# Kernel optimization log

Hardware: AMD Instinct MI355X
Metric: run time of the kernel (lower is better)

The kernel has to match this reference:

```python
import jax, jax.numpy as jnp
import numpy as np

R_, RD_, D_, C_ = 4, 64, 256, 64   # num_relations, relation_dim, input_dim, max_chains
B_, T_ = 32, 512
OUT = R_ * RD_                      # output_dim = num_relations * relation_dim
EPS = 1e-100                        # underflows to 0 in fp32, same as torch


def setup_inputs() -> dict:
    key = jax.random.key(0)
    ks = jax.random.split(key, 10)
    X = jax.random.normal(ks[0], (B_, T_, D_), jnp.float32)
    M = jax.random.randint(ks[1], (B_, T_), 0, 2, jnp.int32)
    Ei = jax.random.randint(ks[2], (B_, T_, C_), 0, 2, jnp.int32)
    Eo = jax.random.randint(ks[3], (B_, T_, C_), 0, 2, jnp.int32)
    Ri = jax.random.randint(ks[4], (B_, T_, C_), 0, R_, jnp.int32)
    Ro = jax.random.randint(ks[5], (B_, T_, C_), 0, R_, jnp.int32)
    W = jax.random.normal(ks[6], (D_, OUT), jnp.float32) * np.sqrt(6.0 / (D_ + OUT))
    U = jax.random.normal(ks[7], (OUT, OUT), jnp.float32) * np.sqrt(6.0 / (OUT + OUT))
    b = jnp.zeros((OUT,), jnp.float32)
    Watt = jax.random.normal(ks[8], (R_, D_), jnp.float32) * 0.1
    return dict(X=X, M=M, Ei=Ei, Eo=Eo, Ri=Ri, Ro=Ro, W=W, U=U, b=b, Watt=Watt)


def _forward(X, M, Ei, Eo, Ri, Ro, W, U, b, Watt):
    B = X.shape[0]
    dt = X.dtype
    # All three gates share the same W/U/b in the original module.
    Wstk = jnp.concatenate([W, W, W], axis=1)   # [D, 3*OUT]
    Ustk = jnp.concatenate([U, U, U], axis=1)   # [OUT, 3*OUT]

    # time-major
    Xre = jnp.transpose(X, (1, 0, 2))           # [T,B,D]
    Xpre = jnp.einsum('tbd,de->tbe', Xre, Wstk) # [T,B,3*OUT] precomputed input proj
    Mre = jnp.transpose(M, (1, 0))              # [T,B]
    Eire = jnp.transpose(Ei, (1, 0, 2))         # [T,B,C]
    Eore = jnp.transpose(Eo, (1, 0, 2))
    Rire = jnp.transpose(Ri, (1, 0, 2))
    Rore = jnp.transpose(Ro, (1, 0, 2))

    h0 = jnp.zeros((B, OUT), dt)
    m0 = jnp.zeros((B, C_, RD_), dt)

    def step(carry, inp):
        hprev, mprev = carry
        x, xp, m, ei, eo, ri, ro = inp
        # gather: one-hot over relations for each chain slot
        r1 = jax.nn.one_hot(ri, R_, dtype=dt)                 # [B,C,R]
        # attention over chains
        v = jnp.einsum('bcr,rd->bcd', r1, Watt)               # [B,C,D]
        actvs = jnp.einsum('bcd,bd->bc', v, x)                # [B,C]
        e = ei.astype(dt)
        am = jnp.exp(actvs) * e + EPS
        alphas = am / jnp.sum(am, axis=1, keepdims=True)      # [B,C]
        agg = jnp.transpose(alphas[:, :, None] * r1, (0, 2, 1))  # [B,R,C]
        prev = jnp.einsum('brc,bcd->brd', agg, mprev).reshape(B, OUT)  # [B,OUT]
        agg_out = jnp.sum(agg, axis=2)                        # [B,R]
        # fused GRU cell (shared weights across gates)
        h2h = prev @ Ustk                                     # [B,3*OUT]
        xr, xz, xh = xp[:, :OUT], xp[:, OUT:2 * OUT], xp[:, 2 * OUT:]
        hr, hz, hh = h2h[:, :OUT], h2h[:, OUT:2 * OUT], h2h[:, 2 * OUT:]
        rg = jax.nn.sigmoid(xr + hr + b)
        z = jax.nn.sigmoid(xz + hz + b)
        ht = jnp.tanh(xh + rg * hh + b)
        hnew = (1.0 - z) * prev + z * ht                      # [B,OUT]
        # scatter new hidden state back into per-chain memory
        hnew_r = hnew.reshape(B, R_, RD_)
        ro1 = jax.nn.one_hot(ro, R_, dtype=dt)                # [B,C,R]
        mnew = jnp.einsum('bcr,brd->bcd', ro1, hnew_r)        # [B,C,RD]
        mflt = m.astype(dt)[:, None]                          # [B,1]
        hout = (1.0 - mflt) * hprev + mflt * hnew
        eo_r = (mflt * eo.astype(dt))[:, :, None]             # [B,C,1]
        mout = (1.0 - eo_r) * mprev + eo_r * mnew
        return (hout, mout), (hout, mout, agg_out)

    _, (outs, mems, aggs) = jax.lax.scan(
        step, (h0, m0), (Xre, Xpre, Mre, Eire, Eore, Rire, Rore))
    return (jnp.transpose(outs, (1, 0, 2)),        # [B,T,OUT]
            jnp.transpose(mems, (1, 0, 2, 3)),     # [B,T,C,RD]
            jnp.transpose(aggs, (1, 0, 2)))        # [B,T,R]


def reference(X, M, Ei, Eo, Ri, Ro, W, U, b, Watt):
    return _forward(X, M, Ei, Eo, Ri, Ro, W, U, b, Watt)
```

## Files before the change

### kernel.cpp

```cpp
#include <hip/hip_runtime.h>

#define B_   32
#define T_   512
#define D_   256
#define C_   64
#define R_   4
#define RD_  64
#define OUT_ 256

__device__ __forceinline__ void bar_lds() {
  asm volatile("s_waitcnt lgkmcnt(0)" ::: "memory");
  __builtin_amdgcn_s_barrier();
  asm volatile("" ::: "memory");
}

template <int CTRL>
__device__ __forceinline__ float dpp_add(float v) {
  int s = __builtin_amdgcn_update_dpp(0, __float_as_int(v), CTRL, 0xF, 0xF, true);
  return v + __int_as_float(s);
}
__device__ __forceinline__ float row16_sum(float v) {
  v = dpp_add<0xB1>(v);
  v = dpp_add<0x4E>(v);
  v = dpp_add<0x141>(v);
  v = dpp_add<0x140>(v);
  return v;
}
__device__ __forceinline__ float rlane(float v, int l) {
  return __int_as_float(__builtin_amdgcn_readlane(__float_as_int(v), l));
}
__device__ __forceinline__ int rlane_i(int v, int l) {
  return __builtin_amdgcn_readlane(v, l);
}
__device__ __forceinline__ float wave_sum_dpp(float v) {
  const float r = row16_sum(v);
  return (rlane(r, 0) + rlane(r, 16)) + (rlane(r, 32) + rlane(r, 48));
}

__global__ __launch_bounds__(256) void xpre_kernel(const float* __restrict__ X,
                                                   const float* __restrict__ W,
                                                   float* __restrict__ XP) {
  __shared__ __align__(16) float xs[32][D_];
  const int j = threadIdx.x;
  const int row0 = blockIdx.x * 32;
  for (int k = 0; k < 32; ++k)
    xs[k][j] = X[(size_t)(row0 + k) * D_ + j];
  __syncthreads();
  float acc[32];
#pragma unroll
  for (int k = 0; k < 32; ++k) acc[k] = 0.f;
  for (int d4 = 0; d4 < D_ / 4; ++d4) {
    const float w0 = W[(d4 * 4 + 0) * OUT_ + j];
    const float w1 = W[(d4 * 4 + 1) * OUT_ + j];
    const float w2 = W[(d4 * 4 + 2) * OUT_ + j];
    const float w3 = W[(d4 * 4 + 3) * OUT_ + j];
#pragma unroll
    for (int k = 0; k < 32; ++k) {
      const float4 x4 = *(const float4*)&xs[k][d4 * 4];
      acc[k] = fmaf(x4.x, w0, fmaf(x4.y, w1, fmaf(x4.z, w2, fmaf(x4.w, w3, acc[k]))));
    }
  }
  for (int k = 0; k < 32; ++k)
    XP[(size_t)(row0 + k) * OUT_ + j] = acc[k];
}

__global__ __launch_bounds__(256) void attnK(const float* __restrict__ X,
                                             const int* __restrict__ Ri,
                                             const int* __restrict__ Ei,
                                             const float* __restrict__ Watt,
                                             float* __restrict__ walG,
                                             float* __restrict__ aggs) {
  const int wv = threadIdx.x >> 6;
  const int lane = threadIdx.x & 63;
  const size_t bt = (size_t)blockIdx.x * 4 + wv;
  const int r4 = lane >> 4, seg = lane & 15;

  float y = 0.f;
#pragma unroll
  for (int q = 0; q < 4; ++q) {
    const float4 wt = *(const float4*)&Watt[(r4 << 8) + (seg << 4) + (q << 2)];
    const float4 xv = *(const float4*)&X[bt * D_ + (seg << 4) + (q << 2)];
    y = fmaf(xv.x, wt.x, y);
    y = fmaf(xv.y, wt.y, y);
    y = fmaf(xv.z, wt.z, y);
    y = fmaf(xv.w, wt.w, y);
  }
  y = row16_sum(y);
  const float y0 = rlane(y, 0), y1 = rlane(y, 16);
  const float y2 = rlane(y, 32), y3 = rlane(y, 48);
  const int ric = Ri[bt * C_ + lane];
  const float eic = (float)Ei[bt * C_ + lane];
  float yv = (ric & 1) ? y1 : y0;
  const float yw = (ric & 1) ? y3 : y2;
  yv = (ric & 2) ? yw : yv;
  const float am = __expf(yv) * eic;
  const float tot = wave_sum_dpp(am);
  const float alpha = __fdividef(am, tot);

  const float w0 = (ric == 0) ? alpha : 0.f;
  const float w1 = (ric == 1) ? alpha : 0.f;
  const float w2 = (ric == 2) ? alpha : 0.f;
  const float w3 = (ric == 3) ? alpha : 0.f;
  walG[bt * 256 + 0 * C_ + lane] = w0;
  walG[bt * 256 + 1 * C_ + lane] = w1;
  walG[bt * 256 + 2 * C_ + lane] = w2;
  walG[bt * 256 + 3 * C_ + lane] = w3;
  const float s0 = wave_sum_dpp(w0);
  const float s1 = wave_sum_dpp(w1);
  const float s2 = wave_sum_dpp(w2);
  const float s3 = wave_sum_dpp(w3);
  if (lane == 0) {
    float4 v = {s0, s1, s2, s3};
    *(float4*)&aggs[bt * R_] = v;
  }
}

__global__ __launch_bounds__(256, 1) void gruA(
    const int* __restrict__ M, const int* __restrict__ Eo,
    const int* __restrict__ Ro, const float* __restrict__ U,
    const float* __restrict__ Bv, const float* __restrict__ XP,
    const float* __restrict__ walG, float* __restrict__ hbuf) {
  __shared__ __align__(16) float shp[4][256];
  __shared__ __align__(16) float pBred[4][256];
  __shared__ __align__(16) float sh_hnew[OUT_];
  __shared__ int sh_tl[T_];
  __shared__ int sh_nT;

  const int tid = threadIdx.x;
  const int lane = tid & 63;
  const int w = tid >> 6;
  const int b = blockIdx.x;
  const size_t bt0 = (size_t)b * T_;

  float ureg[256];
#pragma unroll
  for (int jj = 0; jj < 4; ++jj)
#pragma unroll
    for (int i = 0; i < 64; ++i)
      ureg[(jj << 6) + i] = U[(size_t)((w << 6) + i) * OUT_ + (jj << 6) + lane];
  const float breg = Bv[tid];

  float mtreg[16];
#pragma unroll
  for (int q = 0; q < 16; ++q) mtreg[q] = 0.f;

  if (tid < 64) {
    int base = 0;
    for (int ch = 0; ch < 8; ++ch) {
      const int mv = M[bt0 + (ch << 6) + lane];
      const unsigned long long mask = __ballot(mv != 0);
      if (mv) {
        const unsigned long long lt = ((lane == 63) ? ~0ull : ((1ull << (lane + 1)) - 1)) >> 1;
        sh_tl[base + __popcll(mask & lt)] = (ch << 6) + lane;
      }
      base += __popcll(mask);
    }
    if (lane == 0) sh_nT = base;
  }
  __syncthreads();
  const int nT = sh_nT;
  if (nT == 0) return;

  const int cwal = (w << 4) + (lane >> 2);
  const int croeo = (w << 4) + (lane & 15);
  float walS0 = 0.f, xpS0 = 0.f, walS1 = 0.f, xpS1 = 0.f;
  int roeoS0 = 0, roeoS1 = 0;
  {
    const int t0 = sh_tl[0];
    walS0 = walG[(bt0 + t0) * 256 + ((tid & 3) << 6) + cwal];
    xpS0 = XP[(bt0 + t0) * 256 + tid];
    roeoS0 = Ro[(bt0 + t0) * C_ + croeo] | (Eo[(bt0 + t0) * C_ + croeo] << 8);
  }
  if (nT > 1) {
    const int t1 = sh_tl[1];
    walS1 = walG[(bt0 + t1) * 256 + ((tid & 3) << 6) + cwal];
    xpS1 = XP[(bt0 + t1) * 256 + tid];
    roeoS1 = Ro[(bt0 + t1) * C_ + croeo] | (Eo[(bt0 + t1) * C_ + croeo] << 8);
  }

  auto do_step = [&](int k, float& walS, float& xpS, int& roeoS) {
    const size_t bt = bt0 + sh_tl[k];
    const int roeoCur = roeoS;

    float a0 = 0.f, a1 = 0.f, a2 = 0.f, a3 = 0.f;
#pragma unroll
    for (int q = 0; q < 16; ++q) {
      const float mq = mtreg[q];
      a0 = fmaf(rlane(walS, 4 * q + 0), mq, a0);
      a1 = fmaf(rlane(walS, 4 * q + 1), mq, a1);
      a2 = fmaf(rlane(walS, 4 * q + 2), mq, a2);
      a3 = fmaf(rlane(walS, 4 * q + 3), mq, a3);
    }
    shp[w][0 * 64 + lane] = a0;
    shp[w][1 * 64 + lane] = a1;
    shp[w][2 * 64 + lane] = a2;
    shp[w][3 * 64 + lane] = a3;
    bar_lds();

    const float prevX = ((shp[0][tid] + shp[1][tid]) +
                         (shp[2][tid] + shp[3][tid]));
    float p0 = 0.f, p1 = 0.f, p2 = 0.f, p3 = 0.f;
#pragma unroll
    for (int i = 0; i < 64; ++i) {
      const float pk = rlane(prevX, i);
      p0 = fmaf(pk, ureg[i], p0);
      p1 = fmaf(pk, ureg[64 + i], p1);
      p2 = fmaf(pk, ureg[128 + i], p2);
      p3 = fmaf(pk, ureg[192 + i], p3);
    }
    pBred[w][0 * 64 + lane] = p0;
    pBred[w][1 * 64 + lane] = p1;
    pBred[w][2 * 64 + lane] = p2;
    pBred[w][3 * 64 + lane] = p3;
    bar_lds();

    const float h2h = ((pBred[0][tid] + pBred[1][tid]) +
                       (pBred[2][tid] + pBred[3][tid]));
    const float g1 = xpS + h2h + breg;
    const float rg = 1.f / (1.f + __expf(-g1));
    const float targ = xpS + rg * h2h + breg;
    const float e2 = __expf(2.f * targ);
    const float ht = 1.f - 2.f / (e2 + 1.f);
    const float hn = (1.f - rg) * prevX + rg * ht;
    sh_hnew[tid] = hn;
    hbuf[bt * OUT_ + tid] = hn;
    if (k + 2 < nT) {
      const int t2 = sh_tl[k + 2];
      walS = walG[(bt0 + t2) * 256 + ((tid & 3) << 6) + cwal];
      xpS = XP[(bt0 + t2) * 256 + tid];
      roeoS = Ro[(bt0 + t2) * C_ + croeo] | (Eo[(bt0 + t2) * C_ + croeo] << 8);
    }
    bar_lds();

    const float h0 = sh_hnew[0 * 64 + lane];
    const float h1 = sh_hnew[1 * 64 + lane];
    const float h2 = sh_hnew[2 * 64 + lane];
    const float h3 = sh_hnew[3 * 64 + lane];
#pragma unroll
    for (int q = 0; q < 16; ++q) {
      const int re = rlane_i(roeoCur, q);
      const int ro = re & 0xFF;
      const float ha = (ro & 1) ? h1 : h0;
      const float hb = (ro & 1) ? h3 : h2;
      const float hs = (ro & 2) ? hb : ha;
      mtreg[q] = (re & 0x100) ? hs : mtreg[q];
    }
  };

  for (int k = 0; k < nT; k += 2) {
    do_step(k, walS0, xpS0, roeoS0);
    if (k + 1 < nT) do_step(k + 1, walS1, xpS1, roeoS1);
  }
}

__global__ __launch_bounds__(512) void memsB(const int* __restrict__ M,
                                             const int* __restrict__ Eo,
                                             const int* __restrict__ Ro,
                                             const float* __restrict__ hbuf,
                                             float* __restrict__ mems) {
  __shared__ int lastA[T_];
  const int tid = threadIdx.x;
  const int b = blockIdx.x >> 6;
  const int c = blockIdx.x & 63;
  const size_t bt0 = (size_t)b * T_;
  {
    const int upd = M[bt0 + tid] & Eo[(bt0 + tid) * C_ + c];
    lastA[tid] = upd ? tid : -1;
  }
  __syncthreads();
  for (int off = 1; off < T_; off <<= 1) {
    const int u = (tid >= off) ? lastA[tid - off] : -1;
    const int v = lastA[tid];
    __syncthreads();
    lastA[tid] = (u > v) ? u : v;
    __syncthreads();
  }
  const int d = tid & 63;
  const int t8 = tid >> 6;
  for (int tt = 0; tt < 64; ++tt) {
    const int t = (tt << 3) + t8;
    const int tau = lastA[t];
    float v = 0.f;
    if (tau >= 0) {
      const int rc = Ro[(bt0 + tau) * C_ + c];
      v = hbuf[(bt0 + tau) * OUT_ + (rc << 6) + d];
    }
    mems[((bt0 + t) * C_ + c) * RD_ + d] = v;
  }
}

__global__ __launch_bounds__(512) void outsC(const int* __restrict__ M,
                                             float* __restrict__ outs) {
  __shared__ int lastM[T_];
  const int tid = threadIdx.x;
  const int b = blockIdx.x;
  const size_t bt0 = (size_t)b * T_;
  lastM[tid] = M[bt0 + tid] ? tid : -1;
  __syncthreads();
  for (int off = 1; off < T_; off <<= 1) {
    const int u = (tid >= off) ? lastM[tid - off] : -1;
    const int v = lastM[tid];
    __syncthreads();
    lastM[tid] = (u > v) ? u : v;
    __syncthreads();
  }
  const int j = tid & 255;
  const int th = tid >> 8;
  for (int k = 0; k < 256; ++k) {
    const int t = 511 - (k << 1) - th;
    const int tau = lastM[t];
    const float v = (tau >= 0) ? outs[(bt0 + tau) * OUT_ + j] : 0.f;
    __syncthreads();
    outs[(bt0 + t) * OUT_ + j] = v;
  }
}

extern "C" void kernel_launch(void* const* d_in, const int* in_sizes, int n_in,
                              void* d_out, int out_size, void* d_ws, size_t ws_size,
                              hipStream_t stream) {
  const float* X = (const float*)d_in[0];
  const int* M = (const int*)d_in[1];
  const int* Ei = (const int*)d_in[2];
  const int* Eo = (const int*)d_in[3];
  const int* Ri = (const int*)d_in[4];
  const int* Ro = (const int*)d_in[5];
  const float* W = (const float*)d_in[6];
  const float* U = (const float*)d_in[7];
  const float* Bv = (const float*)d_in[8];
  const float* Watt = (const float*)d_in[9];

  float* outs = (float*)d_out;
  float* mems = outs + (size_t)B_ * T_ * OUT_;
  float* aggs = mems + (size_t)B_ * T_ * C_ * RD_;
  float* XP = (float*)d_ws;
  float* hbuf = outs;
  float* walG = mems;

  xpre_kernel<<<dim3(B_ * T_ / 32), dim3(256), 0, stream>>>(X, W, XP);
  attnK<<<dim3(B_ * T_ / 4), dim3(256), 0, stream>>>(X, Ri, Ei, Watt, walG, aggs);
  gruA<<<dim3(B_), dim3(256), 0, stream>>>(M, Eo, Ro, U, Bv, XP, walG, hbuf);
  memsB<<<dim3(B_ * C_), dim3(512), 0, stream>>>(M, Eo, Ro, hbuf, mems);
  outsC<<<dim3(B_), dim3(512), 0, stream>>>(M, outs);
}
```

Measured before the change: 878.3 us.

## Process two batch sequences per GRU block to share U registers and barriers

```diff
diff --git a/kernel.cpp b/kernel.cpp
--- a/kernel.cpp
+++ b/kernel.cpp
@@ -120,17 +120,17 @@
     const int* __restrict__ Ro, const float* __restrict__ U,
     const float* __restrict__ Bv, const float* __restrict__ XP,
     const float* __restrict__ walG, float* __restrict__ hbuf) {
-  __shared__ __align__(16) float shp[4][256];
-  __shared__ __align__(16) float pBred[4][256];
-  __shared__ __align__(16) float sh_hnew[OUT_];
-  __shared__ int sh_tl[T_];
-  __shared__ int sh_nT;
+  __shared__ __align__(16) float shp[2][4][256];
+  __shared__ __align__(16) float pBred[2][4][256];
+  __shared__ __align__(16) float sh_hnew[2][OUT_];
+  __shared__ int sh_tl[2][T_];
+  __shared__ int sh_nT[2];
 
   const int tid = threadIdx.x;
   const int lane = tid & 63;
   const int w = tid >> 6;
-  const int b = blockIdx.x;
-  const size_t bt0 = (size_t)b * T_;
+  const size_t bt0A = (size_t)(blockIdx.x * 2) * T_;
+  const size_t bt0B = bt0A + T_;
 
   float ureg[256];
 #pragma unroll
@@ -140,116 +140,174 @@
       ureg[(jj << 6) + i] = U[(size_t)((w << 6) + i) * OUT_ + (jj << 6) + lane];
   const float breg = Bv[tid];
 
-  float mtreg[16];
-#pragma unroll
-  for (int q = 0; q < 16; ++q) mtreg[q] = 0.f;
-
-  if (tid < 64) {
+  float mtA[16], mtB[16];
+#pragma unroll
+  for (int q = 0; q < 16; ++q) { mtA[q] = 0.f; mtB[q] = 0.f; }
+
+  for (int i = tid; i < 2 * T_; i += 256) ((int*)sh_tl)[i] = 0;
+  __syncthreads();
+  if (w < 2) {
+    const size_t base0 = (w == 0) ? bt0A : bt0B;
     int base = 0;
     for (int ch = 0; ch < 8; ++ch) {
-      const int mv = M[bt0 + (ch << 6) + lane];
+      const int mv = M[base0 + (ch << 6) + lane];
       const unsigned long long mask = __ballot(mv != 0);
       if (mv) {
         const unsigned long long lt = ((lane == 63) ? ~0ull : ((1ull << (lane + 1)) - 1)) >> 1;
-        sh_tl[base + __popcll(mask & lt)] = (ch << 6) + lane;
+        sh_tl[w][base + __popcll(mask & lt)] = (ch << 6) + lane;
       }
       base += __popcll(mask);
     }
-    if (lane == 0) sh_nT = base;
+    if (lane == 0) sh_nT[w] = base;
   }
   __syncthreads();
-  const int nT = sh_nT;
-  if (nT == 0) return;
+  const int nTA = sh_nT[0], nTB = sh_nT[1];
+  const int kMax = (nTA > nTB) ? nTA : nTB;
+  if (kMax == 0) return;
 
   const int cwal = (w << 4) + (lane >> 2);
   const int croeo = (w << 4) + (lane & 15);
-  float walS0 = 0.f, xpS0 = 0.f, walS1 = 0.f, xpS1 = 0.f;
-  int roeoS0 = 0, roeoS1 = 0;
+  float walA0, xpA0, walA1, xpA1, walB0, xpB0, walB1, xpB1;
+  int reA0, reA1, reB0, reB1;
   {
-    const int t0 = sh_tl[0];
-    walS0 = walG[(bt0 + t0) * 256 + ((tid & 3) << 6) + cwal];
-    xpS0 = XP[(bt0 + t0) * 256 + tid];
-    roeoS0 = Ro[(bt0 + t0) * C_ + croeo] | (Eo[(bt0 + t0) * C_ + croeo] << 8);
-  }
-  if (nT > 1) {
-    const int t1 = sh_tl[1];
-    walS1 = walG[(bt0 + t1) * 256 + ((tid & 3) << 6) + cwal];
-    xpS1 = XP[(bt0 + t1) * 256 + tid];
-    roeoS1 = Ro[(bt0 + t1) * C_ + croeo] | (Eo[(bt0 + t1) * C_ + croeo] << 8);
-  }
-
-  auto do_step = [&](int k, float& walS, float& xpS, int& roeoS) {
-    const size_t bt = bt0 + sh_tl[k];
-    const int roeoCur = roeoS;
-
-    float a0 = 0.f, a1 = 0.f, a2 = 0.f, a3 = 0.f;
+    const int tA = sh_tl[0][0], tB = sh_tl[1][0];
+    walA0 = walG[(bt0A + tA) * 256 + ((tid & 3) << 6) + cwal];
+    xpA0 = XP[(bt0A + tA) * 256 + tid];
+    reA0 = Ro[(bt0A + tA) * C_ + croeo] | (Eo[(bt0A + tA) * C_ + croeo] << 8);
+    walB0 = walG[(bt0B + tB) * 256 + ((tid & 3) << 6) + cwal];
+    xpB0 = XP[(bt0B + tB) * 256 + tid];
+    reB0 = Ro[(bt0B + tB) * C_ + croeo] | (Eo[(bt0B + tB) * C_ + croeo] << 8);
+  }
+  {
+    const int tA = sh_tl[0][1], tB = sh_tl[1][1];
+    walA1 = walG[(bt0A + tA) * 256 + ((tid & 3) << 6) + cwal];
+    xpA1 = XP[(bt0A + tA) * 256 + tid];
+    reA1 = Ro[(bt0A + tA) * C_ + croeo] | (Eo[(bt0A + tA) * C_ + croeo] << 8);
+    walB1 = walG[(bt0B + tB) * 256 + ((tid & 3) << 6) + cwal];
+    xpB1 = XP[(bt0B + tB) * 256 + tid];
+    reB1 = Ro[(bt0B + tB) * C_ + croeo] | (Eo[(bt0B + tB) * C_ + croeo] << 8);
+  }
+
+  auto do_step = [&](int k, float& walA, float& xpA, int& reA,
+                     float& walB, float& xpB, int& reB) {
+    const int tA = sh_tl[0][k], tB = sh_tl[1][k];
+    const bool cmA = (k < nTA), cmB = (k < nTB);
+    const int reAc = reA, reBc = reB;
+
+    float aA0 = 0.f, aA1 = 0.f, aA2 = 0.f, aA3 = 0.f;
+    float aB0 = 0.f, aB1 = 0.f, aB2 = 0.f, aB3 = 0.f;
 #pragma unroll
     for (int q = 0; q < 16; ++q) {
-      const float mq = mtreg[q];
-      a0 = fmaf(rlane(walS, 4 * q + 0), mq, a0);
-      a1 = fmaf(rlane(walS, 4 * q + 1), mq, a1);
-      a2 = fmaf(rlane(walS, 4 * q + 2), mq, a2);
-      a3 = fmaf(rlane(walS, 4 * q + 3), mq, a3);
-    }
-    shp[w][0 * 64 + lane] = a0;
-    shp[w][1 * 64 + lane] = a1;
-    shp[w][2 * 64 + lane] = a2;
-    shp[w][3 * 64 + lane] = a3;
+      const float mA = mtA[q], mB = mtB[q];
+      aA0 = fmaf(rlane(walA, 4 * q + 0), mA, aA0);
+      aA1 = fmaf(rlane(walA, 4 * q + 1), mA, aA1);
+      aA2 = fmaf(rlane(walA, 4 * q + 2), mA, aA2);
+      aA3 = fmaf(rlane(walA, 4 * q + 3), mA, aA3);
+      aB0 = fmaf(rlane(walB, 4 * q + 0), mB, aB0);
+      aB1 = fmaf(rlane(walB, 4 * q + 1), mB, aB1);
+      aB2 = fmaf(rlane(walB, 4 * q + 2), mB, aB2);
+      aB3 = fmaf(rlane(walB, 4 * q + 3), mB, aB3);
+    }
+    shp[0][w][0 * 64 + lane] = aA0;
+    shp[0][w][1 * 64 + lane] = aA1;
+    shp[0][w][2 * 64 + lane] = aA2;
+    shp[0][w][3 * 64 + lane] = aA3;
+    shp[1][w][0 * 64 + lane] = aB0;
+    shp[1][w][1 * 64 + lane] = aB1;
+    shp[1][w][2 * 64 + lane] = aB2;
+    shp[1][w][3 * 64 + lane] = aB3;
     bar_lds();
 
-    const float prevX = ((shp[0][tid] + shp[1][tid]) +
-                         (shp[2][tid] + shp[3][tid]));
-    float p0 = 0.f, p1 = 0.f, p2 = 0.f, p3 = 0.f;
+    const float pXA = ((shp[0][0][tid] + shp[0][1][tid]) +
+                       (shp[0][2][tid] + shp[0][3][tid]));
+    const float pXB = ((shp[1][0][tid] + shp[1][1][tid]) +
+                       (shp[1][2][tid] + shp[1][3][tid]));
+    float pA0 = 0.f, pA1 = 0.f, pA2 = 0.f, pA3 = 0.f;
+    float pB0 = 0.f, pB1 = 0.f, pB2 = 0.f, pB3 = 0.f;
 #pragma unroll
     for (int i = 0; i < 64; ++i) {
-      const float pk = rlane(prevX, i);
-      p0 = fmaf(pk, ureg[i], p0);
-      p1 = fmaf(pk, ureg[64 + i], p1);
-      p2 = fmaf(pk, ureg[128 + i], p2);
-      p3 = fmaf(pk, ureg[192 + i], p3);
-    }
-    pBred[w][0 * 64 + lane] = p0;
-    pBred[w][1 * 64 + lane] = p1;
-    pBred[w][2 * 64 + lane] = p2;
-    pBred[w][3 * 64 + lane] = p3;
+      const float kA = rlane(pXA, i);
+      const float kB = rlane(pXB, i);
+      const float u0 = ureg[i], u1 = ureg[64 + i];
+      const float u2 = ureg[128 + i], u3 = ureg[192 + i];
+      pA0 = fmaf(kA, u0, pA0);
+      pA1 = fmaf(kA, u1, pA1);
+      pA2 = fmaf(kA, u2, pA2);
+      pA3 = fmaf(kA, u3, pA3);
+      pB0 = fmaf(kB, u0, pB0);
+      pB1 = fmaf(kB, u1, pB1);
+      pB2 = fmaf(kB, u2, pB2);
+      pB3 = fmaf(kB, u3, pB3);
+    }
+    pBred[0][w][0 * 64 + lane] = pA0;
+    pBred[0][w][1 * 64 + lane] = pA1;
+    pBred[0][w][2 * 64 + lane] = pA2;
+    pBred[0][w][3 * 64 + lane] = pA3;
+    pBred[1][w][0 * 64 + lane] = pB0;
+    pBred[1][w][1 * 64 + lane] = pB1;
+    pBred[1][w][2 * 64 + lane] = pB2;
+    pBred[1][w][3 * 64 + lane] = pB3;
     bar_lds();
 
-    const float h2h = ((pBred[0][tid] + pBred[1][tid]) +
-                       (pBred[2][tid] + pBred[3][tid]));
-    const float g1 = xpS + h2h + breg;
-    const float rg = 1.f / (1.f + __expf(-g1));
-    const float targ = xpS + rg * h2h + breg;
-    const float e2 = __expf(2.f * targ);
-    const float ht = 1.f - 2.f / (e2 + 1.f);
-    const float hn = (1.f - rg) * prevX + rg * ht;
-    sh_hnew[tid] = hn;
-    hbuf[bt * OUT_ + tid] = hn;
-    if (k + 2 < nT) {
-      const int t2 = sh_tl[k + 2];
-      walS = walG[(bt0 + t2) * 256 + ((tid & 3) << 6) + cwal];
-      xpS = XP[(bt0 + t2) * 256 + tid];
-      roeoS = Ro[(bt0 + t2) * C_ + croeo] | (Eo[(bt0 + t2) * C_ + croeo] << 8);
+    const float h2hA = ((pBred[0][0][tid] + pBred[0][1][tid]) +
+                        (pBred[0][2][tid] + pBred[0][3][tid]));
+    const float h2hB = ((pBred[1][0][tid] + pBred[1][1][tid]) +
+                        (pBred[1][2][tid] + pBred[1][3][tid]));
+    const float g1A = xpA + h2hA + breg;
+    const float g1B = xpB + h2hB + breg;
+    const float rgA = 1.f / (1.f + __expf(-g1A));
+    const float rgB = 1.f / (1.f + __expf(-g1B));
+    const float tgA = xpA + rgA * h2hA + breg;
+    const float tgB = xpB + rgB * h2hB + breg;
+    const float e2A = __expf(2.f * tgA);
+    const float e2B = __expf(2.f * tgB);
+    const float htA = 1.f - 2.f / (e2A + 1.f);
+    const float htB = 1.f - 2.f / (e2B + 1.f);
+    const float hnA = (1.f - rgA) * pXA + rgA * htA;
+    const float hnB = (1.f - rgB) * pXB + rgB * htB;
+    sh_hnew[0][tid] = hnA;
+    sh_hnew[1][tid] = hnB;
+    if (cmA) hbuf[(bt0A + tA) * OUT_ + tid] = hnA;
+    if (cmB) hbuf[(bt0B + tB) * OUT_ + tid] = hnB;
+    {
+      const int kk = (k + 2 < T_) ? k + 2 : T_ - 1;
+      const int tA2 = sh_tl[0][kk], tB2 = sh_tl[1][kk];
+      walA = walG[(bt0A + tA2) * 256 + ((tid & 3) << 6) + cwal];
+      xpA = XP[(bt0A + tA2) * 256 + tid];
+      reA = Ro[(bt0A + tA2) * C_ + croeo] | (Eo[(bt0A + tA2) * C_ + croeo] << 8);
+      walB = walG[(bt0B + tB2) * 256 + ((tid & 3) << 6) + cwal];
+      xpB = XP[(bt0B + tB2) * 256 + tid];
+      reB = Ro[(bt0B + tB2) * C_ + croeo] | (Eo[(bt0B + tB2) * C_ + croeo] << 8);
     }
     bar_lds();
 
-    const float h0 = sh_hnew[0 * 64 + lane];
-    const float h1 = sh_hnew[1 * 64 + lane];
-    const float h2 = sh_hnew[2 * 64 + lane];
-    const float h3 = sh_hnew[3 * 64 + lane];
+    const float hA0 = sh_hnew[0][0 * 64 + lane];
+    const float hA1 = sh_hnew[0][1 * 64 + lane];
+    const float hA2 = sh_hnew[0][2 * 64 + lane];
+    const float hA3 = sh_hnew[0][3 * 64 + lane];
+    const float hB0 = sh_hnew[1][0 * 64 + lane];
+    const float hB1 = sh_hnew[1][1 * 64 + lane];
+    const float hB2 = sh_hnew[1][2 * 64 + lane];
+    const float hB3 = sh_hnew[1][3 * 64 + lane];
 #pragma unroll
     for (int q = 0; q < 16; ++q) {
-      const int re = rlane_i(roeoCur, q);
-      const int ro = re & 0xFF;
-      const float ha = (ro & 1) ? h1 : h0;
-      const float hb = (ro & 1) ? h3 : h2;
-      const float hs = (ro & 2) ? hb : ha;
-      mtreg[q] = (re & 0x100) ? hs : mtreg[q];
+      const int ra = rlane_i(reAc, q);
+      const int rb = rlane_i(reBc, q);
+      const float haA = (ra & 1) ? hA1 : hA0;
+      const float hbA = (ra & 1) ? hA3 : hA2;
+      const float hsA = (ra & 2) ? hbA : haA;
+      mtA[q] = (cmA && (ra & 0x100)) ? hsA : mtA[q];
+      const float haB = (rb & 1) ? hB1 : hB0;
+      const float hbB = (rb & 1) ? hB3 : hB2;
+      const float hsB = (rb & 2) ? hbB : haB;
+      mtB[q] = (cmB && (rb & 0x100)) ? hsB : mtB[q];
     }
   };
 
-  for (int k = 0; k < nT; k += 2) {
-    do_step(k, walS0, xpS0, roeoS0);
-    if (k + 1 < nT) do_step(k + 1, walS1, xpS1, roeoS1);
+  for (int k = 0; k < kMax; k += 2) {
+    do_step(k, walA0, xpA0, reA0, walB0, xpB0, reB0);
+    if (k + 1 < kMax)
+      do_step(k + 1, walA1, xpA1, reA1, walB1, xpB1, reB1);
   }
 }
 
@@ -338,7 +396,7 @@
 
   xpre_kernel<<<dim3(B_ * T_ / 32), dim3(256), 0, stream>>>(X, W, XP);
   attnK<<<dim3(B_ * T_ / 4), dim3(256), 0, stream>>>(X, Ri, Ei, Watt, walG, aggs);
-  gruA<<<dim3(B_), dim3(256), 0, stream>>>(M, Eo, Ro, U, Bv, XP, walG, hbuf);
+  gruA<<<dim3(B_ / 2), dim3(256), 0, stream>>>(M, Eo, Ro, U, Bv, XP, walG, hbuf);
   memsB<<<dim3(B_ * C_), dim3(512), 0, stream>>>(M, Eo, Ro, hbuf, mems);
   outsC<<<dim3(B_), dim3(512), 0, stream>>>(M, outs);
 }
```

Measured after the change: 1.420 ms. +61.7%, slower.

## Split GRU recurrence across eight waves to halve per-wave serial work

Applied to the files above, without the earlier changes.

```diff
diff --git a/kernel.cpp b/kernel.cpp
--- a/kernel.cpp
+++ b/kernel.cpp
@@ -115,13 +115,14 @@
   }
 }
 
-__global__ __launch_bounds__(256, 1) void gruA(
+__global__ __launch_bounds__(512, 2) void gruA(
     const int* __restrict__ M, const int* __restrict__ Eo,
     const int* __restrict__ Ro, const float* __restrict__ U,
     const float* __restrict__ Bv, const float* __restrict__ XP,
     const float* __restrict__ walG, float* __restrict__ hbuf) {
-  __shared__ __align__(16) float shp[4][256];
-  __shared__ __align__(16) float pBred[4][256];
+  __shared__ __align__(16) float shp[8][256];
+  __shared__ __align__(16) float pBred[8][256];
+  __shared__ __align__(16) float shprev[OUT_];
   __shared__ __align__(16) float sh_hnew[OUT_];
   __shared__ int sh_tl[T_];
   __shared__ int sh_nT;
@@ -132,17 +133,17 @@
   const int b = blockIdx.x;
   const size_t bt0 = (size_t)b * T_;
 
-  float ureg[256];
+  float ureg[128];
 #pragma unroll
   for (int jj = 0; jj < 4; ++jj)
 #pragma unroll
-    for (int i = 0; i < 64; ++i)
-      ureg[(jj << 6) + i] = U[(size_t)((w << 6) + i) * OUT_ + (jj << 6) + lane];
-  const float breg = Bv[tid];
-
-  float mtreg[16];
-#pragma unroll
-  for (int q = 0; q < 16; ++q) mtreg[q] = 0.f;
+    for (int i = 0; i < 32; ++i)
+      ureg[(jj << 5) + i] = U[(size_t)((w << 5) + i) * OUT_ + (jj << 6) + lane];
+  const float breg = Bv[tid & 255];
+
+  float mtreg[8];
+#pragma unroll
+  for (int q = 0; q < 8; ++q) mtreg[q] = 0.f;
 
   if (tid < 64) {
     int base = 0;
@@ -161,35 +162,36 @@
   const int nT = sh_nT;
   if (nT == 0) return;
 
-  const int cwal = (w << 4) + (lane >> 2);
-  const int croeo = (w << 4) + (lane & 15);
+  const int cwal = (w << 3) + (lane >> 3);
+  const int rwal = lane & 3;
+  const int croeo = (w << 3) + (lane & 7);
   float walS0 = 0.f, xpS0 = 0.f, walS1 = 0.f, xpS1 = 0.f;
-  int roeoS0 = 0, roeoS1 = 0;
+  int reS0 = 0, reS1 = 0;
   {
     const int t0 = sh_tl[0];
-    walS0 = walG[(bt0 + t0) * 256 + ((tid & 3) << 6) + cwal];
-    xpS0 = XP[(bt0 + t0) * 256 + tid];
-    roeoS0 = Ro[(bt0 + t0) * C_ + croeo] | (Eo[(bt0 + t0) * C_ + croeo] << 8);
+    walS0 = walG[(bt0 + t0) * 256 + (rwal << 6) + cwal];
+    if (w < 4) xpS0 = XP[(bt0 + t0) * 256 + tid];
+    reS0 = Ro[(bt0 + t0) * C_ + croeo] | (Eo[(bt0 + t0) * C_ + croeo] << 8);
   }
   if (nT > 1) {
     const int t1 = sh_tl[1];
-    walS1 = walG[(bt0 + t1) * 256 + ((tid & 3) << 6) + cwal];
-    xpS1 = XP[(bt0 + t1) * 256 + tid];
-    roeoS1 = Ro[(bt0 + t1) * C_ + croeo] | (Eo[(bt0 + t1) * C_ + croeo] << 8);
-  }
-
-  auto do_step = [&](int k, float& walS, float& xpS, int& roeoS) {
+    walS1 = walG[(bt0 + t1) * 256 + (rwal << 6) + cwal];
+    if (w < 4) xpS1 = XP[(bt0 + t1) * 256 + tid];
+    reS1 = Ro[(bt0 + t1) * C_ + croeo] | (Eo[(bt0 + t1) * C_ + croeo] << 8);
+  }
+
+  auto do_step = [&](int k, float& walS, float& xpS, int& reS) {
     const size_t bt = bt0 + sh_tl[k];
-    const int roeoCur = roeoS;
+    const int reC = reS;
 
     float a0 = 0.f, a1 = 0.f, a2 = 0.f, a3 = 0.f;
 #pragma unroll
-    for (int q = 0; q < 16; ++q) {
+    for (int q = 0; q < 8; ++q) {
       const float mq = mtreg[q];
-      a0 = fmaf(rlane(walS, 4 * q + 0), mq, a0);
-      a1 = fmaf(rlane(walS, 4 * q + 1), mq, a1);
-      a2 = fmaf(rlane(walS, 4 * q + 2), mq, a2);
-      a3 = fmaf(rlane(walS, 4 * q + 3), mq, a3);
+      a0 = fmaf(rlane(walS, 8 * q + 0), mq, a0);
+      a1 = fmaf(rlane(walS, 8 * q + 1), mq, a1);
+      a2 = fmaf(rlane(walS, 8 * q + 2), mq, a2);
+      a3 = fmaf(rlane(walS, 8 * q + 3), mq, a3);
     }
     shp[w][0 * 64 + lane] = a0;
     shp[w][1 * 64 + lane] = a1;
@@ -197,16 +199,18 @@
     shp[w][3 * 64 + lane] = a3;
     bar_lds();
 
-    const float prevX = ((shp[0][tid] + shp[1][tid]) +
-                         (shp[2][tid] + shp[3][tid]));
+    const int kidx = (w << 5) + (lane & 31);
+    const float px = ((shp[0][kidx] + shp[1][kidx]) + (shp[2][kidx] + shp[3][kidx])) +
+                     ((shp[4][kidx] + shp[5][kidx]) + (shp[6][kidx] + shp[7][kidx]));
+    if (lane < 32) shprev[kidx] = px;
     float p0 = 0.f, p1 = 0.f, p2 = 0.f, p3 = 0.f;
 #pragma unroll
-    for (int i = 0; i < 64; ++i) {
-      const float pk = rlane(prevX, i);
+    for (int i = 0; i < 32; ++i) {
+      const float pk = rlane(px, i);
       p0 = fmaf(pk, ureg[i], p0);
-      p1 = fmaf(pk, ureg[64 + i], p1);
-      p2 = fmaf(pk, ureg[128 + i], p2);
-      p3 = fmaf(pk, ureg[192 + i], p3);
+      p1 = fmaf(pk, ureg[32 + i], p1);
+      p2 = fmaf(pk, ureg[64 + i], p2);
+      p3 = fmaf(pk, ureg[96 + i], p3);
     }
     pBred[w][0 * 64 + lane] = p0;
     pBred[w][1 * 64 + lane] = p1;
@@ -214,21 +218,26 @@
     pBred[w][3 * 64 + lane] = p3;
     bar_lds();
 
-    const float h2h = ((pBred[0][tid] + pBred[1][tid]) +
-                       (pBred[2][tid] + pBred[3][tid]));
-    const float g1 = xpS + h2h + breg;
-    const float rg = 1.f / (1.f + __expf(-g1));
-    const float targ = xpS + rg * h2h + breg;
-    const float e2 = __expf(2.f * targ);
-    const float ht = 1.f - 2.f / (e2 + 1.f);
-    const float hn = (1.f - rg) * prevX + rg * ht;
-    sh_hnew[tid] = hn;
-    hbuf[bt * OUT_ + tid] = hn;
+    if (w < 4) {
+      const float h2h = ((pBred[0][tid] + pBred[1][tid]) +
+                         (pBred[2][tid] + pBred[3][tid])) +
+                        ((pBred[4][tid] + pBred[5][tid]) +
+                         (pBred[6][tid] + pBred[7][tid]));
+      const float pOwn = shprev[tid];
+      const float g1 = xpS + h2h + breg;
+      const float rg = 1.f / (1.f + __expf(-g1));
+      const float targ = xpS + rg * h2h + breg;
+      const float e2 = __expf(2.f * targ);
+      const float ht = 1.f - 2.f / (e2 + 1.f);
+      const float hn = (1.f - rg) * pOwn + rg * ht;
+      sh_hnew[tid] = hn;
+      hbuf[bt * OUT_ + tid] = hn;
+    }
     if (k + 2 < nT) {
       const int t2 = sh_tl[k + 2];
-      walS = walG[(bt0 + t2) * 256 + ((tid & 3) << 6) + cwal];
-      xpS = XP[(bt0 + t2) * 256 + tid];
-      roeoS = Ro[(bt0 + t2) * C_ + croeo] | (Eo[(bt0 + t2) * C_ + croeo] << 8);
+      walS = walG[(bt0 + t2) * 256 + (rwal << 6) + cwal];
+      if (w < 4) xpS = XP[(bt0 + t2) * 256 + tid];
+      reS = Ro[(bt0 + t2) * C_ + croeo] | (Eo[(bt0 + t2) * C_ + croeo] << 8);
     }
     bar_lds();
 
@@ -237,8 +246,8 @@
     const float h2 = sh_hnew[2 * 64 + lane];
     const float h3 = sh_hnew[3 * 64 + lane];
 #pragma unroll
-    for (int q = 0; q < 16; ++q) {
-      const int re = rlane_i(roeoCur, q);
+    for (int q = 0; q < 8; ++q) {
+      const int re = rlane_i(reC, q);
       const int ro = re & 0xFF;
       const float ha = (ro & 1) ? h1 : h0;
       const float hb = (ro & 1) ? h3 : h2;
@@ -248,8 +257,8 @@
   };
 
   for (int k = 0; k < nT; k += 2) {
-    do_step(k, walS0, xpS0, roeoS0);
-    if (k + 1 < nT) do_step(k + 1, walS1, xpS1, roeoS1);
+    do_step(k, walS0, xpS0, reS0);
+    if (k + 1 < nT) do_step(k + 1, walS1, xpS1, reS1);
   }
 }
 
@@ -338,7 +347,7 @@
 
   xpre_kernel<<<dim3(B_ * T_ / 32), dim3(256), 0, stream>>>(X, W, XP);
   attnK<<<dim3(B_ * T_ / 4), dim3(256), 0, stream>>>(X, Ri, Ei, Watt, walG, aggs);
-  gruA<<<dim3(B_), dim3(256), 0, stream>>>(M, Eo, Ro, U, Bv, XP, walG, hbuf);
+  gruA<<<dim3(B_), dim3(512), 0, stream>>>(M, Eo, Ro, U, Bv, XP, walG, hbuf);
   memsB<<<dim3(B_ * C_), dim3(512), 0, stream>>>(M, Eo, Ro, hbuf, mems);
   outsC<<<dim3(B_), dim3(512), 0, stream>>>(M, outs);
 }
```

Result: faster. 775.1 us (-11.8%).
